# Performance work log

Hardware: AMD Instinct MI355X
Metric: run time of the kernel (lower is better)

The kernel has to match this reference:

```python
import jax, jax.numpy as jnp
import numpy as np

D = 512
H = 8
HD = D // H
EPS = 1e-8


def setup_inputs() -> dict:
    key = jax.random.key(0)
    ks = jax.random.split(key, 16)
    B, S = 4, 2048
    s = lambda n: 1.0 / np.sqrt(n)
    inp = {
        "gene_emb": jax.random.normal(ks[0], (B, S, D), jnp.float32),
        "expr_emb": jax.random.normal(ks[1], (B, S, D), jnp.float32),
        "M": jax.random.uniform(ks[2], (B, S, S), jnp.float32),
        # weights stored (in, out) so y = x @ W + b
        "W_fused": jax.random.normal(ks[3], (2 * D, D), jnp.float32) * s(2 * D),
        "b_fused": jnp.zeros((D,), jnp.float32),
        "W_Q": jax.random.normal(ks[4], (D, D), jnp.float32) * s(D),
        "b_Q": jnp.zeros((D,), jnp.float32),
        "W_K": jax.random.normal(ks[5], (D, D), jnp.float32) * s(D),
        "b_K": jnp.zeros((D,), jnp.float32),
        "W_V": jax.random.normal(ks[6], (D, D), jnp.float32) * s(D),
        "b_V": jnp.zeros((D,), jnp.float32),
        "W_O": jax.random.normal(ks[7], (D, D), jnp.float32) * s(D),
        "b_O": jnp.zeros((D,), jnp.float32),
    }
    return inp


def reference(gene_emb, expr_emb, M, W_fused, b_fused, W_Q, b_Q, W_K, b_K, W_V, b_V, W_O, b_O):
    B, S, _ = gene_emb.shape
    scale = HD ** (-0.5)
    fused = jnp.concatenate([gene_emb, expr_emb], axis=-1) @ W_fused + b_fused
    # (B,S,D) -> (B,H,S,HD)
    split = lambda x: x.reshape(B, S, H, HD).transpose(0, 2, 1, 3)
    Q = split(fused @ W_Q + b_Q)
    K = split(fused @ W_K + b_K)
    V = split(expr_emb @ W_V + b_V)
    scores = jnp.einsum("bhqd,bhkd->bhqk", Q, K) * scale
    Mg = M[:, None, :, :]  # broadcast over heads
    scores = scores * Mg
    attn = jax.nn.softmax(scores, axis=-1)
    A_sparse = attn * Mg
    norm = jnp.sum(jnp.abs(A_sparse), axis=-1, keepdims=True) + EPS
    A_bar = A_sparse / norm
    out = jnp.einsum("bhqk,bhkd->bhqd", A_bar, V)
    out = out.transpose(0, 2, 1, 3).reshape(B, S, D)
    return out @ W_O + b_O
```

## Files before the change

kernel.cpp:

```cpp
#include <hip/hip_runtime.h>

typedef unsigned short u16;
typedef __attribute__((ext_vector_type(8))) short bf16x8_t;
typedef __attribute__((ext_vector_type(4))) float f32x4_t;
typedef __attribute__((ext_vector_type(16))) float f32x16_t;

__device__ __forceinline__ u16 f2bf(float x){
  union { float f; unsigned u; } v; v.f = x;
  unsigned r = v.u + 0x7FFFu + ((v.u >> 16) & 1u);
  return (u16)(r >> 16);
}
__device__ __forceinline__ float bf2f(u16 h){
  union { unsigned u; float f; } v; v.u = ((unsigned)h) << 16;
  return v.f;
}
__device__ __forceinline__ unsigned pack_hi16(float a, float b){
  union { float f; unsigned u; } x, y; x.f = a; y.f = b;
  return (x.u >> 16) | (y.u & 0xFFFF0000u);
}

__device__ __forceinline__ void gl2lds16(const u16* g, u16* l){
  __builtin_amdgcn_global_load_lds((const __attribute__((address_space(1))) void*)g,
                                   (__attribute__((address_space(3))) void*)l, 16, 0, 0);
}

__global__ __launch_bounds__(256) void split_concat_kernel(
    const float* __restrict__ gene, const float* __restrict__ expr,
    u16* __restrict__ Xh, u16* __restrict__ Xl)
{
  size_t e = ((size_t)blockIdx.x * 256 + threadIdx.x) * 4;
  int row = (int)(e >> 10);
  int col = (int)(e & 1023);
  const float* src = (col < 512) ? (gene + (size_t)row * 512 + col)
                                 : (expr + (size_t)row * 512 + (col - 512));
  float4 v = *(const float4*)src;
  float a[4] = {v.x, v.y, v.z, v.w};
  u16 hs[4], ls[4];
#pragma unroll
  for (int i = 0; i < 4; i++){
    hs[i] = f2bf(a[i]);
    ls[i] = f2bf(a[i] - bf2f(hs[i]));
  }
  *(uint2*)(Xh + e) = make_uint2(hs[0] | ((unsigned)hs[1] << 16), hs[2] | ((unsigned)hs[3] << 16));
  *(uint2*)(Xl + e) = make_uint2(ls[0] | ((unsigned)ls[1] << 16), ls[2] | ((unsigned)ls[3] << 16));
}

__global__ __launch_bounds__(256) void transpose_all_kernel(
    const float* __restrict__ Wf, const float* __restrict__ Wq,
    const float* __restrict__ Wk, const float* __restrict__ Wv,
    const float* __restrict__ Wo,
    u16* __restrict__ Wfth, u16* __restrict__ Wftl,
    u16* __restrict__ Wqth, u16* __restrict__ Wkth,
    u16* __restrict__ Wvth, u16* __restrict__ Woth)
{
  __shared__ float t[64][65];
  int id = blockIdx.x;
  const float* W; u16* Th; u16* Tl; int K, kx, ny;
  if (id < 128){ W = Wf; Th = Wfth; Tl = Wftl; K = 1024; kx = id >> 3; ny = id & 7; }
  else {
    int tt = id - 128; int wi = tt >> 6; tt &= 63; kx = tt >> 3; ny = tt & 7; K = 512;
    W  = (wi == 0) ? Wq  : (wi == 1) ? Wk  : (wi == 2) ? Wv  : Wo;
    Th = (wi == 0) ? Wqth: (wi == 1) ? Wkth: (wi == 2) ? Wvth: Woth;
    Tl = nullptr;
  }
  int k0 = kx * 64, n0 = ny * 64;
  int tid = threadIdx.x;
  int r = tid >> 4;
  int c4 = (tid & 15) * 4;
#pragma unroll
  for (int p = 0; p < 4; p++){
    int k = p * 16 + r;
    float4 v = *(const float4*)(W + (size_t)(k0 + k) * 512 + n0 + c4);
    t[c4 + 0][k] = v.x; t[c4 + 1][k] = v.y; t[c4 + 2][k] = v.z; t[c4 + 3][k] = v.w;
  }
  __syncthreads();
#pragma unroll
  for (int p = 0; p < 4; p++){
    int n = p * 16 + r;
    u16 hs[4], ls[4];
#pragma unroll
    for (int i = 0; i < 4; i++){
      float x = t[n][c4 + i];
      hs[i] = f2bf(x);
      ls[i] = f2bf(x - bf2f(hs[i]));
    }
    size_t o = (size_t)(n0 + n) * K + k0 + c4;
    *(uint2*)(Th + o) = make_uint2(hs[0] | ((unsigned)hs[1] << 16), hs[2] | ((unsigned)hs[3] << 16));
    if (Tl)
      *(uint2*)(Tl + o) = make_uint2(ls[0] | ((unsigned)ls[1] << 16), ls[2] | ((unsigned)ls[3] << 16));
  }
}

template<int SPLITS, int MODE, int DUAL>
__global__ __launch_bounds__(256, 2) void gemm_kernel(
    const u16* __restrict__ Ah, const u16* __restrict__ Al, int lda,
    const u16* __restrict__ Bh0, const u16* __restrict__ Bl0,
    const u16* __restrict__ Bh1, int K,
    const float* __restrict__ bias0, const float* __restrict__ bias1,
    void* __restrict__ out0, void* __restrict__ out1, void* __restrict__ outsec,
    float sc0, float sc1)
{
  __shared__ __align__(16) u16 sAh[2][128 * 32];
  __shared__ __align__(16) u16 sAl[SPLITS >= 2 ? 2 : 1][SPLITS >= 2 ? 128 * 32 : 8];
  __shared__ __align__(16) u16 sBh[2][64 * 32];
  __shared__ __align__(16) u16 sBl[SPLITS == 3 ? 2 : 1][SPLITS == 3 ? 64 * 32 : 8];
  int tid = threadIdx.x;
  int lane = tid & 63, w = tid >> 6, quad = lane >> 4, l15 = lane & 15;
  int wm = w & 1, wn = w >> 1;
  int lid = (int)(blockIdx.y * gridDim.x + blockIdx.x);
  int side = DUAL ? (lid >> 9) : 0;
  int l = lid & 511;
  int m0 = (((l & 7) << 3) | ((l >> 3) & 7)) * 128;
  int n0 = (l >> 6) * 64;
  const u16* Bh = (DUAL && side) ? Bh1 : Bh0;
  const float* bias = (DUAL && side) ? bias1 : bias0;
  void* o0 = (DUAL && side) ? outsec : out0;
  float sc = (DUAL && side) ? sc1 : sc0;

  f32x4_t acc[4][2];
#pragma unroll
  for (int i = 0; i < 4; i++)
#pragma unroll
    for (int j = 0; j < 2; j++)
#pragma unroll
      for (int r = 0; r < 4; r++) acc[i][j][r] = 0.f;

  int lrow = lane >> 2;
  int swzS = ((lane >> 2) & 3) ^ ((lane >> 4) & 3);
  int gkq  = ((lane & 3) ^ swzS) * 8;
  const u16* pAh0 = Ah + (size_t)(m0 + w * 32 + lrow) * lda + gkq;
  const u16* pAh1 = Ah + (size_t)(m0 + w * 32 + 16 + lrow) * lda + gkq;
  const u16* pAl0 = (SPLITS >= 2) ? Al + (size_t)(m0 + w * 32 + lrow) * lda + gkq : nullptr;
  const u16* pAl1 = (SPLITS >= 2) ? Al + (size_t)(m0 + w * 32 + 16 + lrow) * lda + gkq : nullptr;
  const u16* pBh0 = Bh + (size_t)(n0 + w * 16 + lrow) * K + gkq;
  const u16* pBl0 = (SPLITS == 3) ? Bl0 + (size_t)(n0 + w * 16 + lrow) * K + gkq : nullptr;

  int pq = (quad ^ ((l15 & 3) ^ ((l15 >> 2) & 3))) * 8;

#define STAGEG(B, KK) do {                                                 \
    gl2lds16(pAh0 + (KK), &sAh[B][w * 1024]);                              \
    gl2lds16(pAh1 + (KK), &sAh[B][w * 1024 + 512]);                        \
    if constexpr (SPLITS >= 2){                                            \
      gl2lds16(pAl0 + (KK), &sAl[B][w * 1024]);                            \
      gl2lds16(pAl1 + (KK), &sAl[B][w * 1024 + 512]);                      \
    }                                                                      \
    gl2lds16(pBh0 + (KK), &sBh[B][w * 512]);                               \
    if constexpr (SPLITS == 3)                                             \
      gl2lds16(pBl0 + (KK), &sBl[B][w * 512]);                             \
  } while (0)

  STAGEG(0, 0);
  __syncthreads();

  int T = K >> 5;
  for (int t = 0; t < T; ++t){
    int ph = t & 1;
    bool nx = (t + 1) < T;
    if (nx) STAGEG(ph ^ 1, (t + 1) * 32);

    bf16x8_t aH[4], aL[4], bH[2], bL[2];
#pragma unroll
    for (int mi = 0; mi < 4; mi++){
      int ad = (wm * 64 + mi * 16 + l15) * 32 + pq;
      aH[mi] = *(const bf16x8_t*)&sAh[ph][ad];
      if constexpr (SPLITS >= 2) aL[mi] = *(const bf16x8_t*)&sAl[ph][ad];
    }
#pragma unroll
    for (int ni = 0; ni < 2; ni++){
      int bd = (wn * 32 + ni * 16 + l15) * 32 + pq;
      bH[ni] = *(const bf16x8_t*)&sBh[ph][bd];
      if constexpr (SPLITS == 3) bL[ni] = *(const bf16x8_t*)&sBl[ph][bd];
    }
#pragma unroll
    for (int mi = 0; mi < 4; mi++)
#pragma unroll
      for (int ni = 0; ni < 2; ni++){
        acc[mi][ni] = __builtin_amdgcn_mfma_f32_16x16x32_bf16(aH[mi], bH[ni], acc[mi][ni], 0, 0, 0);
        if constexpr (SPLITS == 3)
          acc[mi][ni] = __builtin_amdgcn_mfma_f32_16x16x32_bf16(aH[mi], bL[ni], acc[mi][ni], 0, 0, 0);
        if constexpr (SPLITS >= 2)
          acc[mi][ni] = __builtin_amdgcn_mfma_f32_16x16x32_bf16(aL[mi], bH[ni], acc[mi][ni], 0, 0, 0);
      }

    if (nx) __syncthreads();
  }
#undef STAGEG

#pragma unroll
  for (int mi = 0; mi < 4; mi++)
#pragma unroll
    for (int ni = 0; ni < 2; ni++){
      int gn = n0 + wn * 32 + ni * 16 + l15;
      float bs = bias[gn];
      int gm0 = m0 + wm * 64 + mi * 16 + quad * 4;
#pragma unroll
      for (int r = 0; r < 4; r++){
        float v = acc[mi][ni][r] + bs;
        int gm = gm0 + r;
        if constexpr (MODE == 0){
          u16 hb = f2bf(v);
          ((u16*)o0)[(size_t)gm * 512 + gn] = hb;
          ((u16*)out1)[(size_t)gm * 512 + gn] = f2bf(v - bf2f(hb));
        } else if constexpr (MODE == 1){
          ((u16*)o0)[(size_t)gm * 512 + gn] = f2bf(v * sc);
        } else if constexpr (MODE == 2){
          int bb = gm >> 11, s = gm & 2047;
          int hh = gn >> 6, d = gn & 63;
          ((u16*)o0)[((size_t)((bb * 8 + hh) * 64 + d) << 11) + s] = f2bf(v);
        } else {
          ((float*)o0)[(size_t)gm * 512 + gn] = v;
        }
      }
    }
}

__global__ __launch_bounds__(256, 2) void flash_kernel(
    const u16* __restrict__ Qh, const u16* __restrict__ Kh,
    const u16* __restrict__ Vt, const float* __restrict__ Mm,
    u16* __restrict__ Oh)
{
  __shared__ __align__(16) u16 sAll[2][16384];
  int tid = threadIdx.x, lane = tid & 63, w = tid >> 6;
  int ql = lane & 31, hi = lane >> 5;
  int wq = w >> 1, wk = w & 1;
  int by = blockIdx.y, b = by >> 2, h0 = (by & 3) * 2;
  int q0 = blockIdx.x * 64;
  int q  = q0 + wq * 32 + ql;

  const u16* qp = Qh + ((size_t)(b * 2048 + q)) * 512 + h0 * 64 + hi * 8;
  bf16x8_t qf[2][4];
#pragma unroll
  for (int h = 0; h < 2; h++)
#pragma unroll
    for (int dt = 0; dt < 4; dt++)
      qf[h][dt] = *(const bf16x8_t*)(qp + h * 64 + dt * 16);

  int srow = lane >> 3, c8 = lane & 7;
  const u16* gK[4]; const u16* gV[4];
#pragma unroll
  for (int c = 0; c < 4; c++){
    int kv = wk * 32 + c * 8 + srow;
    int skey = ((c >> 1) << 2) | ((c & 1) << 1) | (srow & 1);
    gK[c] = Kh + ((size_t)(b * 2048 + kv)) * 512 + (h0 + wq) * 64 + ((c8 ^ skey) << 3);
    gV[c] = Vt + ((size_t)((b * 8 + h0 + wq) * 64 + kv)) * 2048 + ((c8 ^ srow) << 3);
  }
  int dO = wq * 4096 + wk * 2048;

  int phi = ((ql >> 3) & 1) * 16 + ((ql >> 2) & 1) * 8 + (ql >> 4) * 4 + (ql & 3);
  int kvL = wk * 32 + phi;
  int skr = ((ql >> 3) & 1) * 4 + ((ql >> 2) & 1) * 2 + (ql & 1);
  int kaddr[4];
#pragma unroll
  for (int dt = 0; dt < 4; dt++)
    kaddr[dt] = kvL * 64 + (((dt * 2 + hi) ^ skr) << 3);
  int vaddr[2][2];
#pragma unroll
  for (int dn = 0; dn < 2; dn++)
#pragma unroll
    for (int kt = 0; kt < 2; kt++)
      vaddr[dn][kt] = (dn * 32 + ql) * 64 + (((wk * 4 + kt * 2 + hi) ^ (ql & 7)) << 3);

  const float* mp = Mm + (size_t)b * (2048 * 2048) + (size_t)q * 2048 + wk * 32 + hi * 8;
  const int og[4] = {0, 16, 4, 20};

  float lp[2] = {0.f, 0.f};
  f32x16_t Oc[2][2];
#pragma unroll
  for (int h = 0; h < 2; h++)
#pragma unroll
    for (int dn = 0; dn < 2; dn++)
#pragma unroll
      for (int r = 0; r < 16; r++) Oc[h][dn][r] = 0.f;

#define STAGE(B, KK) do {                                              \
    _Pragma("unroll")                                                  \
    for (int c = 0; c < 4; c++){                                       \
      gl2lds16(gK[c] + (size_t)(KK) * 512, &sAll[B][dO + c * 512]);    \
      gl2lds16(gV[c] + (KK),               &sAll[B][8192 + dO + c * 512]); \
    }                                                                  \
  } while (0)

  STAGE(0, 0);
  f32x4_t Mc[4], Mn[4];
#pragma unroll
  for (int g = 0; g < 4; g++) Mc[g] = *(const f32x4_t*)(mp + og[g]);
  __syncthreads();

  for (int t = 0; t < 32; ++t){
    int ph = t & 1;
    bool nx = t < 31;
    if (nx) STAGE(ph ^ 1, (t + 1) * 64);
    if (nx){
#pragma unroll
      for (int g = 0; g < 4; g++) Mn[g] = *(const f32x4_t*)(mp + (t + 1) * 64 + og[g]);
    }
    const u16* kb = &sAll[ph][0];
    const u16* vb = &sAll[ph][8192];

#pragma unroll
    for (int h = 0; h < 2; ++h){
      const u16* kbh = kb + h * 4096;
      const u16* vbh = vb + h * 4096;

      f32x16_t S;
#pragma unroll
      for (int r = 0; r < 16; r++) S[r] = 0.f;
#pragma unroll
      for (int dt = 0; dt < 4; dt++){
        bf16x8_t kf = *(const bf16x8_t*)&kbh[kaddr[dt]];
        S = __builtin_amdgcn_mfma_f32_32x32x16_bf16(kf, qf[h][dt], S, 0, 0, 0);
      }

      float p[16];
#pragma unroll
      for (int g = 0; g < 4; g++)
#pragma unroll
        for (int e = 0; e < 4; e++){
          float m = Mc[g][e];
          float v = m * __builtin_amdgcn_exp2f(S[g * 4 + e] * m);
          lp[h] += v;
          p[g * 4 + e] = v;
        }
#pragma unroll
      for (int kt = 0; kt < 2; kt++){
        union { unsigned u[4]; bf16x8_t v8; } pb;
        pb.u[0] = pack_hi16(p[kt * 4 + 0], p[kt * 4 + 1]);
        pb.u[1] = pack_hi16(p[kt * 4 + 2], p[kt * 4 + 3]);
        pb.u[2] = pack_hi16(p[kt * 4 + 8], p[kt * 4 + 9]);
        pb.u[3] = pack_hi16(p[kt * 4 + 10], p[kt * 4 + 11]);
#pragma unroll
        for (int dn = 0; dn < 2; dn++){
          bf16x8_t vf = *(const bf16x8_t*)&vbh[vaddr[dn][kt]];
          Oc[h][dn] = __builtin_amdgcn_mfma_f32_32x32x16_bf16(vf, pb.v8, Oc[h][dn], 0, 0, 0);
        }
      }
    }

    __syncthreads();
    if (nx){
#pragma unroll
      for (int g = 0; g < 4; g++) Mc[g] = Mn[g];
    }
  }
#undef STAGE

  lp[0] += __shfl_xor(lp[0], 32);
  lp[1] += __shfl_xor(lp[1], 32);

  float* red = (float*)&sAll[0][0];
  float* lpr = red + 8192;
  if (wk){
#pragma unroll
    for (int h = 0; h < 2; h++){
#pragma unroll
      for (int dn = 0; dn < 2; dn++)
#pragma unroll
        for (int rq = 0; rq < 4; rq++){
          f32x4_t o;
          o[0] = Oc[h][dn][rq * 4 + 0]; o[1] = Oc[h][dn][rq * 4 + 1];
          o[2] = Oc[h][dn][rq * 4 + 2]; o[3] = Oc[h][dn][rq * 4 + 3];
          *(f32x4_t*)&red[((((wq * 2 + h) * 2 + dn) * 4 + rq) * 64 + lane) * 4] = o;
        }
      lpr[(wq * 2 + h) * 64 + lane] = lp[h];
    }
  }
  __syncthreads();
  if (!wk){
#pragma unroll
    for (int h = 0; h < 2; h++){
      float li = lp[h] + lpr[(wq * 2 + h) * 64 + lane];
      float inv = 1.0f / li;
      size_t ob = ((size_t)(b * 2048 + q)) * 512 + (h0 + h) * 64;
#pragma unroll
      for (int dn = 0; dn < 2; dn++)
#pragma unroll
        for (int rq = 0; rq < 4; rq++){
          f32x4_t o = *(const f32x4_t*)&red[((((wq * 2 + h) * 2 + dn) * 4 + rq) * 64 + lane) * 4];
          float v0 = (Oc[h][dn][rq * 4 + 0] + o[0]) * inv;
          float v1 = (Oc[h][dn][rq * 4 + 1] + o[1]) * inv;
          float v2 = (Oc[h][dn][rq * 4 + 2] + o[2]) * inv;
          float v3 = (Oc[h][dn][rq * 4 + 3] + o[3]) * inv;
          int d0 = dn * 32 + rq * 8 + hi * 4;
          unsigned w0 = (unsigned)f2bf(v0) | ((unsigned)f2bf(v1) << 16);
          unsigned w1 = (unsigned)f2bf(v2) | ((unsigned)f2bf(v3) << 16);
          *(uint2*)(Oh + ob + d0) = make_uint2(w0, w1);
        }
    }
  }
}

extern "C" void kernel_launch(void* const* d_in, const int* in_sizes, int n_in,
                              void* d_out, int out_size, void* d_ws, size_t ws_size,
                              hipStream_t stream)
{
  const float* gene = (const float*)d_in[0];
  const float* expr = (const float*)d_in[1];
  const float* Mm   = (const float*)d_in[2];
  const float* Wf   = (const float*)d_in[3];
  const float* bfv  = (const float*)d_in[4];
  const float* Wq   = (const float*)d_in[5];
  const float* bq   = (const float*)d_in[6];
  const float* Wk   = (const float*)d_in[7];
  const float* bk   = (const float*)d_in[8];
  const float* Wv   = (const float*)d_in[9];
  const float* bv   = (const float*)d_in[10];
  const float* Wo   = (const float*)d_in[11];
  const float* bo   = (const float*)d_in[12];
  float* out = (float*)d_out;

  char* ws = (char*)d_ws;
  size_t off = 0;
  auto alloc = [&](size_t bytes) -> void* {
    void* p = (void*)(ws + off);
    off += (bytes + 255) & ~(size_t)255;
    return p;
  };
  u16* Xh   = (u16*)alloc(8192ull * 1024 * 2);
  u16* Xl   = (u16*)alloc(8192ull * 1024 * 2);
  u16* Wfth = (u16*)alloc(512ull * 1024 * 2);
  u16* Wftl = (u16*)alloc(512ull * 1024 * 2);
  u16* Wqth = (u16*)alloc(512ull * 512 * 2);
  u16* Wkth = (u16*)alloc(512ull * 512 * 2);
  u16* Wvth = (u16*)alloc(512ull * 512 * 2);
  u16* Woth = (u16*)alloc(512ull * 512 * 2);
  u16* Fh   = (u16*)alloc(8192ull * 512 * 2);
  u16* Fl   = (u16*)alloc(8192ull * 512 * 2);
  u16* Qh   = (u16*)alloc(8192ull * 512 * 2);
  u16* Kh   = (u16*)alloc(8192ull * 512 * 2);
  u16* Vt   = (u16*)alloc(8192ull * 512 * 2);
  u16* Oh = Xh;

  const float QSC = 0.1803368801f;

  split_concat_kernel<<<8192, 256, 0, stream>>>(gene, expr, Xh, Xl);
  transpose_all_kernel<<<384, 256, 0, stream>>>(Wf, Wq, Wk, Wv, Wo,
                                                Wfth, Wftl, Wqth, Wkth, Wvth, Woth);

  gemm_kernel<3, 0, 0><<<dim3(64, 8), 256, 0, stream>>>(
      Xh, Xl, 1024, Wfth, Wftl, nullptr, 1024, bfv, nullptr, Fh, Fl, nullptr, 1.f, 1.f);
  gemm_kernel<2, 1, 1><<<dim3(64, 16), 256, 0, stream>>>(
      Fh, Fl, 512, Wqth, nullptr, Wkth, 512, bq, bk, Qh, nullptr, Kh, QSC, 1.f);
  gemm_kernel<2, 2, 0><<<dim3(64, 8), 256, 0, stream>>>(
      Xh + 512, Xl + 512, 1024, Wvth, nullptr, nullptr, 512, bv, nullptr, Vt, nullptr, nullptr, 1.f, 1.f);
  flash_kernel<<<dim3(32, 16), 256, 0, stream>>>(Qh, Kh, Vt, Mm, Oh);
  gemm_kernel<1, 3, 0><<<dim3(64, 8), 256, 0, stream>>>(
      Oh, nullptr, 512, Woth, nullptr, nullptr, 512, bo, nullptr, out, nullptr, nullptr, 1.f, 1.f);

  (void)in_sizes; (void)n_in; (void)out_size; (void)ws_size;
}
```

Measured before the change: 301.4 us.

## Fold fused projection into Q/K weights and merge QKV into one GEMM

Result: slower. 359.2 us (+19.2%).

```diff
diff --git a/kernel.cpp b/kernel.cpp
--- a/kernel.cpp
+++ b/kernel.cpp
@@ -45,24 +45,16 @@
   *(uint2*)(Xl + e) = make_uint2(ls[0] | ((unsigned)ls[1] << 16), ls[2] | ((unsigned)ls[3] << 16));
 }
 
-__global__ __launch_bounds__(256) void transpose_all_kernel(
-    const float* __restrict__ Wf, const float* __restrict__ Wq,
-    const float* __restrict__ Wk, const float* __restrict__ Wv,
-    const float* __restrict__ Wo,
-    u16* __restrict__ Wfth, u16* __restrict__ Wftl,
-    u16* __restrict__ Wqth, u16* __restrict__ Wkth,
+__global__ __launch_bounds__(256) void transpose_vo_kernel(
+    const float* __restrict__ Wv, const float* __restrict__ Wo,
     u16* __restrict__ Wvth, u16* __restrict__ Woth)
 {
   __shared__ float t[64][65];
   int id = blockIdx.x;
-  const float* W; u16* Th; u16* Tl; int K, kx, ny;
-  if (id < 128){ W = Wf; Th = Wfth; Tl = Wftl; K = 1024; kx = id >> 3; ny = id & 7; }
-  else {
-    int tt = id - 128; int wi = tt >> 6; tt &= 63; kx = tt >> 3; ny = tt & 7; K = 512;
-    W  = (wi == 0) ? Wq  : (wi == 1) ? Wk  : (wi == 2) ? Wv  : Wo;
-    Th = (wi == 0) ? Wqth: (wi == 1) ? Wkth: (wi == 2) ? Wvth: Woth;
-    Tl = nullptr;
-  }
+  const float* W = (id < 64) ? Wv : Wo;
+  u16* Th = (id < 64) ? Wvth : Woth;
+  int tt = id & 63;
+  int kx = tt >> 3, ny = tt & 7;
   int k0 = kx * 64, n0 = ny * 64;
   int tid = threadIdx.x;
   int r = tid >> 4;
@@ -77,18 +69,189 @@
 #pragma unroll
   for (int p = 0; p < 4; p++){
     int n = p * 16 + r;
-    u16 hs[4], ls[4];
-#pragma unroll
-    for (int i = 0; i < 4; i++){
-      float x = t[n][c4 + i];
-      hs[i] = f2bf(x);
-      ls[i] = f2bf(x - bf2f(hs[i]));
-    }
-    size_t o = (size_t)(n0 + n) * K + k0 + c4;
+    u16 hs[4];
+#pragma unroll
+    for (int i = 0; i < 4; i++) hs[i] = f2bf(t[n][c4 + i]);
+    size_t o = (size_t)(n0 + n) * 512 + k0 + c4;
     *(uint2*)(Th + o) = make_uint2(hs[0] | ((unsigned)hs[1] << 16), hs[2] | ((unsigned)hs[3] << 16));
-    if (Tl)
-      *(uint2*)(Tl + o) = make_uint2(ls[0] | ((unsigned)ls[1] << 16), ls[2] | ((unsigned)ls[3] << 16));
-  }
+  }
+}
+
+__global__ __launch_bounds__(256) void wcomp_kernel(
+    const float* __restrict__ Wf, const float* __restrict__ Wq,
+    const float* __restrict__ Wk, u16* __restrict__ Bqt, u16* __restrict__ Bkt)
+{
+  __shared__ float tF[64][65];
+  __shared__ float tW[64][65];
+  int bid = blockIdx.x;
+  int mat = bid >> 7, rest = bid & 127;
+  int kt = rest >> 3, nt = rest & 7;
+  const float* Wx = mat ? Wk : Wq;
+  u16* Bt = mat ? Bkt : Bqt;
+  int k0 = kt * 64, n0 = nt * 64;
+  int tid = threadIdx.x;
+  int r = tid >> 4, c4 = (tid & 15) * 4;
+  int tk = (tid >> 4) * 4, tn = (tid & 15) * 4;
+
+  float acc[4][4];
+#pragma unroll
+  for (int a = 0; a < 4; a++)
+#pragma unroll
+    for (int b = 0; b < 4; b++) acc[a][b] = 0.f;
+
+  for (int j0 = 0; j0 < 512; j0 += 64){
+    __syncthreads();
+#pragma unroll
+    for (int p = 0; p < 4; p++){
+      int row = p * 16 + r;
+      float4 a = *(const float4*)(Wf + (size_t)(k0 + row) * 512 + j0 + c4);
+      *(float4*)&tF[row][c4] = a;
+      float4 b = *(const float4*)(Wx + (size_t)(j0 + row) * 512 + n0 + c4);
+      *(float4*)&tW[row][c4] = b;
+    }
+    __syncthreads();
+#pragma unroll 8
+    for (int jj = 0; jj < 64; jj++){
+      float fa0 = tF[tk + 0][jj], fa1 = tF[tk + 1][jj];
+      float fa2 = tF[tk + 2][jj], fa3 = tF[tk + 3][jj];
+      float4 wb = *(const float4*)&tW[jj][tn];
+      acc[0][0] += fa0 * wb.x; acc[0][1] += fa0 * wb.y; acc[0][2] += fa0 * wb.z; acc[0][3] += fa0 * wb.w;
+      acc[1][0] += fa1 * wb.x; acc[1][1] += fa1 * wb.y; acc[1][2] += fa1 * wb.z; acc[1][3] += fa1 * wb.w;
+      acc[2][0] += fa2 * wb.x; acc[2][1] += fa2 * wb.y; acc[2][2] += fa2 * wb.z; acc[2][3] += fa2 * wb.w;
+      acc[3][0] += fa3 * wb.x; acc[3][1] += fa3 * wb.y; acc[3][2] += fa3 * wb.z; acc[3][3] += fa3 * wb.w;
+    }
+  }
+#pragma unroll
+  for (int b = 0; b < 4; b++){
+    u16 h0 = f2bf(acc[0][b]), h1 = f2bf(acc[1][b]);
+    u16 h2 = f2bf(acc[2][b]), h3 = f2bf(acc[3][b]);
+    *(uint2*)(Bt + (size_t)(n0 + tn + b) * 1024 + k0 + tk) =
+        make_uint2(h0 | ((unsigned)h1 << 16), h2 | ((unsigned)h3 << 16));
+  }
+}
+
+__global__ __launch_bounds__(256) void bcomp_kernel(
+    const float* __restrict__ Wq, const float* __restrict__ Wk,
+    const float* __restrict__ bfv, const float* __restrict__ bq,
+    const float* __restrict__ bk, float* __restrict__ bq2, float* __restrict__ bk2)
+{
+  int mat = blockIdx.x;
+  const float* W = mat ? Wk : Wq;
+  const float* bb = mat ? bk : bq;
+  float* ob = mat ? bk2 : bq2;
+  int tid = threadIdx.x;
+  for (int n = tid; n < 512; n += 256){
+    float a = bb[n];
+    for (int j = 0; j < 512; j++)
+      a += bfv[j] * W[(size_t)j * 512 + n];
+    ob[n] = a;
+  }
+}
+
+__global__ __launch_bounds__(256, 3) void qkv_kernel(
+    const u16* __restrict__ Xh, const u16* __restrict__ Xl,
+    const u16* __restrict__ Bq, const u16* __restrict__ Bk, const u16* __restrict__ Bv,
+    const float* __restrict__ bq2, const float* __restrict__ bk2, const float* __restrict__ bv,
+    u16* __restrict__ Qh, u16* __restrict__ Kh, u16* __restrict__ Vt, float qsc)
+{
+  __shared__ __align__(16) u16 sAh[2][4096];
+  __shared__ __align__(16) u16 sAl[2][4096];
+  __shared__ __align__(16) u16 sBh[2][2048];
+  int tid = threadIdx.x;
+  int lane = tid & 63, w = tid >> 6, quad = lane >> 4, l15 = lane & 15;
+  int wm = w & 1, wn = w >> 1;
+  int lid = (int)(blockIdx.y * gridDim.x + blockIdx.x);
+  int side = lid >> 9;
+  int l = lid & 511;
+  int m0 = (((l & 7) << 3) | ((l >> 3) & 7)) * 128;
+  int n0 = (l >> 6) * 64;
+  const u16* Bh = (side == 0) ? Bq : (side == 1) ? Bk : Bv;
+  const float* bias = (side == 0) ? bq2 : (side == 1) ? bk2 : bv;
+  int K = (side == 2) ? 512 : 1024;
+  int aoff = (side == 2) ? 512 : 0;
+  float sc = (side == 0) ? qsc : 1.f;
+
+  f32x4_t acc[4][2];
+#pragma unroll
+  for (int i = 0; i < 4; i++)
+#pragma unroll
+    for (int j = 0; j < 2; j++)
+#pragma unroll
+      for (int r = 0; r < 4; r++) acc[i][j][r] = 0.f;
+
+  int lrow = lane >> 2;
+  int swzS = ((lane >> 2) & 3) ^ ((lane >> 4) & 3);
+  int gkq  = ((lane & 3) ^ swzS) * 8;
+  const u16* pAh0 = Xh + (size_t)(m0 + w * 32 + lrow) * 1024 + aoff + gkq;
+  const u16* pAh1 = Xh + (size_t)(m0 + w * 32 + 16 + lrow) * 1024 + aoff + gkq;
+  const u16* pAl0 = Xl + (size_t)(m0 + w * 32 + lrow) * 1024 + aoff + gkq;
+  const u16* pAl1 = Xl + (size_t)(m0 + w * 32 + 16 + lrow) * 1024 + aoff + gkq;
+  const u16* pBh0 = Bh + (size_t)(n0 + w * 16 + lrow) * K + gkq;
+
+  int pq = (quad ^ ((l15 & 3) ^ ((l15 >> 2) & 3))) * 8;
+
+#define STAGEQ(B, KK) do {                                                 \
+    gl2lds16(pAh0 + (KK), &sAh[B][w * 1024]);                              \
+    gl2lds16(pAh1 + (KK), &sAh[B][w * 1024 + 512]);                        \
+    gl2lds16(pAl0 + (KK), &sAl[B][w * 1024]);                              \
+    gl2lds16(pAl1 + (KK), &sAl[B][w * 1024 + 512]);                        \
+    gl2lds16(pBh0 + (KK), &sBh[B][w * 512]);                               \
+  } while (0)
+
+  STAGEQ(0, 0);
+  __syncthreads();
+
+  int T = K >> 5;
+  for (int t = 0; t < T; ++t){
+    int ph = t & 1;
+    bool nx = (t + 1) < T;
+    if (nx) STAGEQ(ph ^ 1, (t + 1) * 32);
+
+    bf16x8_t aH[4], aL[4], bH[2];
+#pragma unroll
+    for (int mi = 0; mi < 4; mi++){
+      int ad = (wm * 64 + mi * 16 + l15) * 32 + pq;
+      aH[mi] = *(const bf16x8_t*)&sAh[ph][ad];
+      aL[mi] = *(const bf16x8_t*)&sAl[ph][ad];
+    }
+#pragma unroll
+    for (int ni = 0; ni < 2; ni++){
+      int bd = (wn * 32 + ni * 16 + l15) * 32 + pq;
+      bH[ni] = *(const bf16x8_t*)&sBh[ph][bd];
+    }
+#pragma unroll
+    for (int mi = 0; mi < 4; mi++)
+#pragma unroll
+      for (int ni = 0; ni < 2; ni++){
+        acc[mi][ni] = __builtin_amdgcn_mfma_f32_16x16x32_bf16(aH[mi], bH[ni], acc[mi][ni], 0, 0, 0);
+        acc[mi][ni] = __builtin_amdgcn_mfma_f32_16x16x32_bf16(aL[mi], bH[ni], acc[mi][ni], 0, 0, 0);
+      }
+
+    if (nx) __syncthreads();
+  }
+#undef STAGEQ
+
+  u16* out = (side == 0) ? Qh : (side == 1) ? Kh : Vt;
+#pragma unroll
+  for (int mi = 0; mi < 4; mi++)
+#pragma unroll
+    for (int ni = 0; ni < 2; ni++){
+      int gn = n0 + wn * 32 + ni * 16 + l15;
+      float bs = bias[gn];
+      int gm0 = m0 + wm * 64 + mi * 16 + quad * 4;
+#pragma unroll
+      for (int r = 0; r < 4; r++){
+        float v = acc[mi][ni][r] + bs;
+        int gm = gm0 + r;
+        if (side < 2){
+          out[(size_t)gm * 512 + gn] = f2bf(v * sc);
+        } else {
+          int bb = gm >> 11, s = gm & 2047;
+          int hh = gn >> 6, d = gn & 63;
+          out[((size_t)((bb * 8 + hh) * 64 + d) << 11) + s] = f2bf(v);
+        }
+      }
+    }
 }
 
 template<int SPLITS, int MODE, int DUAL>
@@ -417,14 +580,12 @@
   };
   u16* Xh   = (u16*)alloc(8192ull * 1024 * 2);
   u16* Xl   = (u16*)alloc(8192ull * 1024 * 2);
-  u16* Wfth = (u16*)alloc(512ull * 1024 * 2);
-  u16* Wftl = (u16*)alloc(512ull * 1024 * 2);
-  u16* Wqth = (u16*)alloc(512ull * 512 * 2);
-  u16* Wkth = (u16*)alloc(512ull * 512 * 2);
   u16* Wvth = (u16*)alloc(512ull * 512 * 2);
   u16* Woth = (u16*)alloc(512ull * 512 * 2);
-  u16* Fh   = (u16*)alloc(8192ull * 512 * 2);
-  u16* Fl   = (u16*)alloc(8192ull * 512 * 2);
+  u16* Bqt  = (u16*)alloc(512ull * 1024 * 2);
+  u16* Bkt  = (u16*)alloc(512ull * 1024 * 2);
+  float* bq2 = (float*)alloc(512 * 4);
+  float* bk2 = (float*)alloc(512 * 4);
   u16* Qh   = (u16*)alloc(8192ull * 512 * 2);
   u16* Kh   = (u16*)alloc(8192ull * 512 * 2);
   u16* Vt   = (u16*)alloc(8192ull * 512 * 2);
@@ -433,15 +594,11 @@
   const float QSC = 0.1803368801f;
 
   split_concat_kernel<<<8192, 256, 0, stream>>>(gene, expr, Xh, Xl);
-  transpose_all_kernel<<<384, 256, 0, stream>>>(Wf, Wq, Wk, Wv, Wo,
-                                                Wfth, Wftl, Wqth, Wkth, Wvth, Woth);
-
-  gemm_kernel<3, 0, 0><<<dim3(64, 8), 256, 0, stream>>>(
-      Xh, Xl, 1024, Wfth, Wftl, nullptr, 1024, bfv, nullptr, Fh, Fl, nullptr, 1.f, 1.f);
-  gemm_kernel<2, 1, 1><<<dim3(64, 16), 256, 0, stream>>>(
-      Fh, Fl, 512, Wqth, nullptr, Wkth, 512, bq, bk, Qh, nullptr, Kh, QSC, 1.f);
-  gemm_kernel<2, 2, 0><<<dim3(64, 8), 256, 0, stream>>>(
-      Xh + 512, Xl + 512, 1024, Wvth, nullptr, nullptr, 512, bv, nullptr, Vt, nullptr, nullptr, 1.f, 1.f);
+  transpose_vo_kernel<<<128, 256, 0, stream>>>(Wv, Wo, Wvth, Woth);
+  wcomp_kernel<<<256, 256, 0, stream>>>(Wf, Wq, Wk, Bqt, Bkt);
+  bcomp_kernel<<<2, 256, 0, stream>>>(Wq, Wk, bfv, bq, bk, bq2, bk2);
+  qkv_kernel<<<dim3(64, 24), 256, 0, stream>>>(
+      Xh, Xl, Bqt, Bkt, Wvth, bq2, bk2, bv, Qh, Kh, Vt, QSC);
   flash_kernel<<<dim3(32, 16), 256, 0, stream>>>(Qh, Kh, Vt, Mm, Oh);
   gemm_kernel<1, 3, 0><<<dim3(64, 8), 256, 0, stream>>>(
       Oh, nullptr, 512, Woth, nullptr, nullptr, 512, bo, nullptr, out, nullptr, nullptr, 1.f, 1.f);
```
